# Optimization experiments

Hardware: AMD Instinct MI355X
Metric: run time of the kernel (lower is better)

The kernel has to match this reference:

```python
import jax, jax.numpy as jnp
import numpy as np

N = 50000          # nodes
E = 1_600_000      # edges (avg degree 32)
F = 64             # num_features
IN = 8             # in_channels per band
BANDS = F // IN    # 8 band passes
H = 2              # heads
C = 16             # mid_channels (per-head dim)
HC = H * C         # 32
GIN = HC * BANDS   # 256, GCNConv input dim
OUT = 32           # out_channels
ELU_ALPHA = 0.1


def setup_inputs() -> dict:
    key = jax.random.key(0)
    ks = jax.random.split(key, 12)
    s = 0.05
    inp = {
        "x": jax.random.normal(ks[0], (N, F), jnp.float32),
        "edge_attrs": jax.random.uniform(ks[1], (E, 2), jnp.float32),
        # TransformerConv linear layers (shared across all band passes)
        "Wq": jax.random.normal(ks[2], (IN, HC), jnp.float32) * s,
        "bq": jnp.zeros((HC,), jnp.float32),
        "Wk": jax.random.normal(ks[3], (IN, HC), jnp.float32) * s,
        "bk": jnp.zeros((HC,), jnp.float32),
        "Wv": jax.random.normal(ks[4], (IN, HC), jnp.float32) * s,
        "bv": jnp.zeros((HC,), jnp.float32),
        "We": jax.random.normal(ks[5], (2, HC), jnp.float32) * s,   # lin_edge, no bias
        "Wskip": jax.random.normal(ks[6], (IN, HC), jnp.float32) * s,
        "bskip": jnp.zeros((HC,), jnp.float32),
        # final GCNConv (improved=True)
        "Wg": jax.random.normal(ks[7], (GIN, OUT), jnp.float32) * s,
        "bg": jnp.zeros((OUT,), jnp.float32),
        "edge_index": jax.random.randint(ks[8], (2, E), 0, N, jnp.int32),
    }
    return inp


def reference(x, edge_attrs, Wq, bq, Wk, bk, Wv, bv, We, Wskip, bskip, Wg, bg, edge_index):
    src, dst = edge_index[0], edge_index[1]
    inv_sqrt_c = 1.0 / jnp.sqrt(jnp.float32(C))

    # edge embedding is band-independent; compute once
    e = (edge_attrs @ We).reshape(E, H, C)

    def band_pass(xi):  # xi: [N, IN]
        q = (xi @ Wq + bq).reshape(N, H, C)
        k = (xi @ Wk + bk).reshape(N, H, C)
        v = (xi @ Wv + bv).reshape(N, H, C)
        kj = k[src] + e                                   # [E,H,C]
        logits = jnp.einsum('ehc,ehc->eh', q[dst], kj) * inv_sqrt_c
        # segment softmax over incoming edges of each dst node
        m = jax.ops.segment_max(logits, dst, num_segments=N)
        m = jnp.where(jnp.isfinite(m), m, 0.0)
        p = jnp.exp(logits - m[dst])
        z = jax.ops.segment_sum(p, dst, num_segments=N)
        alpha = p / (z[dst] + 1e-16)                      # [E,H]
        msg = (v[src] + e) * alpha[:, :, None]            # [E,H,C]
        agg = jax.ops.segment_sum(msg, dst, num_segments=N).reshape(N, HC)
        out = agg + xi @ Wskip + bskip                    # root/skip connection
        # GraphMid applies ELU(alpha=0.1) after the conv
        return jnp.where(out > 0, out, ELU_ALPHA * (jnp.exp(out) - 1.0))

    xb = x.reshape(N, BANDS, IN)
    h = jax.vmap(band_pass, in_axes=1, out_axes=1)(xb).reshape(N, GIN)

    # GCNConv(improved=True) with edge_weight = edge_attrs[:, 1]
    w = edge_attrs[:, 1]
    loops = jnp.arange(N, dtype=src.dtype)
    row = jnp.concatenate([src, loops])
    col = jnp.concatenate([dst, loops])
    ww = jnp.concatenate([w, jnp.full((N,), 2.0, jnp.float32)])  # improved: fill=2
    deg = jax.ops.segment_sum(ww, col, num_segments=N)
    dis = jnp.where(deg > 0, jax.lax.rsqrt(deg), 0.0)
    norm = dis[row] * ww * dis[col]                       # [E+N]
    hw = h @ Wg                                           # [N,OUT]
    out = jax.ops.segment_sum(norm[:, None] * hw[row], col, num_segments=N) + bg
    return out
```

## Files before the change

kernel.cpp:

```cpp
#include <hip/hip_runtime.h>
#include <hip/hip_fp16.h>
#include <math.h>

#define NN 50000
#define NE 1600000
#define F 64
#define H 2
#define C 16
#define HC 32
#define GIN 256
#define OUTC 32
#define PAD 88

#define NPART 196
#define CAPP 9216
#define EPB 8192
#define NB1 196
#define QKV_BLOCKS 1563

static const size_t OFF_QH   = 0;
static const size_t OFF_SH   = (size_t)NN * 128;
static const size_t OFF_KV   = 2 * (size_t)NN * 128;
static const size_t OFF_HWH  = OFF_KV + (size_t)NN * 128;
static const size_t OFF_DIS  = OFF_HWH + (size_t)NN * 16;
static const size_t OFF_CUR  = OFF_DIS + NN;
static const size_t OFF_PCUR = OFF_CUR + NN;
static const size_t OFF_PART = OFF_PCUR + 4096;
static const size_t OFF_PAY  = OFF_PART + (size_t)NPART * CAPP * 2;

typedef _Float16 h2 __attribute__((ext_vector_type(2)));
typedef _Float16 h4 __attribute__((ext_vector_type(4)));
typedef _Float16 h8 __attribute__((ext_vector_type(8)));
typedef float f2 __attribute__((ext_vector_type(2)));
union F4H { float4 f; h2 h[4]; };
union H8U { h8 v; h2 h[4]; };
union I2H { int2 i; h2 h[2]; };

__device__ __forceinline__ float fdot2(h2 a, h2 b, float c) {
#if defined(__has_builtin) && __has_builtin(__builtin_amdgcn_fdot2)
    return __builtin_amdgcn_fdot2(a, b, c, false);
#else
    return c + (float)a.x * (float)b.x + (float)a.y * (float)b.y;
#endif
}

__device__ __forceinline__ h2 dec_lo(unsigned d) {
    union { unsigned u; h2 h; } c;
    c.u = __builtin_amdgcn_perm(d, d, 0x010C000CU);
    return c.h;
}
__device__ __forceinline__ h2 dec_hi(unsigned d) {
    union { unsigned u; h2 h; } c;
    c.u = __builtin_amdgcn_perm(d, d, 0x030C020CU);
    return c.h;
}

#if defined(__has_builtin)
#if __has_builtin(__builtin_amdgcn_cvt_pk_f32_bf8)
#define HAVE_CVT_BF8 1
#endif
#endif

__device__ __forceinline__ f2 bf8_lo(int w) {
#ifdef HAVE_CVT_BF8
    return __builtin_amdgcn_cvt_pk_f32_bf8(w, false);
#else
    h2 hh = dec_lo((unsigned)w);
    float2 f = __half22float2(*(const __half2*)&hh);
    f2 r; r.x = f.x; r.y = f.y; return r;
#endif
}
__device__ __forceinline__ f2 bf8_hi(int w) {
#ifdef HAVE_CVT_BF8
    return __builtin_amdgcn_cvt_pk_f32_bf8(w, true);
#else
    h2 hh = dec_hi((unsigned)w);
    float2 f = __half22float2(*(const __half2*)&hh);
    f2 r; r.x = f.x; r.y = f.y; return r;
#endif
}

__global__ __launch_bounds__(256) void k_init(int* __restrict__ pcur) {
    int t = threadIdx.x;
    for (int i = t; i < 4096; i += 256) pcur[i] = 0;
}

__global__ __launch_bounds__(256) void k_p1(
    const float* __restrict__ x,
    const float* __restrict__ Wq, const float* __restrict__ bq,
    const float* __restrict__ Wk, const float* __restrict__ bk,
    const float* __restrict__ Wv, const float* __restrict__ bv,
    const float* __restrict__ Wskip, const float* __restrict__ bskip,
    __half* __restrict__ Qh, unsigned char* __restrict__ KV8,
    __half* __restrict__ Sh,
    const int* __restrict__ ei, const float* __restrict__ ea,
    int* __restrict__ pcur, int2* __restrict__ partA) {
    __shared__ float xs[32 * F];
    __shared__ int hist[256];
    __shared__ int basep[256];
    int t = threadIdx.x;
    if (blockIdx.x < NB1) {
        hist[t] = 0;
        __syncthreads();
        int e0 = blockIdx.x * EPB + t;
        for (int r = 0; r < EPB / 256; r++) {
            int e = e0 + r * 256;
            if (e < NE) atomicAdd(&hist[ei[NE + e] >> 8], 1);
        }
        __syncthreads();
        {
            int c = hist[t];
            basep[t] = (t < NPART && c > 0) ? atomicAdd(pcur + t * 16, c) : 0;
            hist[t] = 0;
        }
        __syncthreads();
        for (int r = 0; r < EPB / 256; r++) {
            int e = e0 + r * 256;
            if (e < NE) {
                int s = ei[e];
                int d = ei[NE + e];
                float2 a = ((const float2*)ea)[e];
                int bin = d >> 8;
                int loff = atomicAdd(&hist[bin], 1);
                int g = basep[bin] + loff;
                if (g < CAPP) {
                    __half2 eh = __floats2half2_rn(a.x, a.y);
                    int2 rec;
                    rec.x = (s & 0xFFFF) | ((d & 255) << 16);
                    rec.y = *(const int*)&eh;
                    partA[(size_t)bin * CAPP + g] = rec;
                }
            }
        }
        return;
    }
    int base = (blockIdx.x - NB1) * 32;
    for (int i = t; i < 32 * F; i += 256) {
        int node = base + (i >> 6);
        xs[i] = (node < NN) ? x[node * F + (i & 63)] : 0.0f;
    }
    __syncthreads();
    int j = t;
    int band = j >> 5;
    int hc = j & 31;
    float wq[8], wk[8], wv[8], ws[8];
#pragma unroll
    for (int i = 0; i < 8; i++) {
        wq[i] = Wq[i * HC + hc];
        wk[i] = Wk[i * HC + hc];
        wv[i] = Wv[i * HC + hc];
        ws[i] = Wskip[i * HC + hc];
    }
    float bq_ = bq[hc], bk_ = bk[hc], bv_ = bv[hc], bs_ = bskip[hc];
    int bh = j >> 4, ch = j & 15;
    int sub = ch >> 2, pos = ch & 3;
    size_t kvoff = (size_t)bh * 32 + (size_t)sub * 8 + pos;
    for (int nn = 0; nn < 32; nn++) {
        int node = base + nn;
        if (node >= NN) break;
        const float* xr = &xs[nn * F + band * 8];
        float q = bq_, k = bk_, v = bv_, s = bs_;
#pragma unroll
        for (int i = 0; i < 8; i++) {
            float xv = xr[i];
            q += xv * wq[i];
            k += xv * wk[i];
            v += xv * wv[i];
            s += xv * ws[i];
        }
        Qh[(size_t)node * 256 + j] = __float2half(q);
        Sh[(size_t)node * 256 + j] = __float2half(s);
        unsigned ku = __half_as_ushort(__float2half(k));
        unsigned vu = __half_as_ushort(__float2half(v));
        KV8[(size_t)node * 512 + kvoff]     = (unsigned char)((ku + 0x80u) >> 8);
        KV8[(size_t)node * 512 + kvoff + 4] = (unsigned char)((vu + 0x80u) >> 8);
    }
}

__global__ __launch_bounds__(256) void k_p2(
    const int* __restrict__ pcur, const int2* __restrict__ partA,
    int2* __restrict__ pay, int* __restrict__ cur) {
    __shared__ int lcnt[256];
    int p = blockIdx.x;
    int t = threadIdx.x;
    lcnt[t] = 0;
    __syncthreads();
    int nrec = pcur[p * 16];
    if (nrec > CAPP) nrec = CAPP;
    const int2* pb = partA + (size_t)p * CAPP;
    for (int i = t; i < nrec; i += 256) {
        int2 rec = pb[i];
        int s = rec.x & 0xFFFF;
        int d8 = (rec.x >> 16) & 255;
        int pos = atomicAdd(&lcnt[d8], 1);
        if (pos < PAD) {
            int2 pl;
            pl.x = s;
            pl.y = rec.y;
            pay[(size_t)((p << 8) + d8) * PAD + pos] = pl;
        }
    }
    __syncthreads();
    int d = (p << 8) + t;
    if (d < NN) cur[d] = lcnt[t];
}

__global__ __launch_bounds__(256) void k_agg(
    const unsigned char* __restrict__ KV8, const __half* __restrict__ Sh,
    const float* __restrict__ We, const float* __restrict__ Wg,
    const int* __restrict__ cnt, const int2* __restrict__ pay,
    const __half* __restrict__ QH,
    __half* __restrict__ HWh, float* __restrict__ dis) {
    __shared__ __attribute__((aligned(16))) _Float16 wgt[32][264];
    __shared__ __attribute__((aligned(16))) _Float16 hls[4][256];
    int t = threadIdx.x;
    for (int idx = t; idx < GIN * OUTC; idx += 256)
        wgt[idx & 31][idx >> 5] = (_Float16)Wg[idx];

    int wv = t >> 6;
    int n = __builtin_amdgcn_readfirstlane(blockIdx.x * 4 + wv);
    int lane = t & 63;
    int bh = lane >> 2;
    int sub = lane & 3;
    int head = bh & 1;
    int coff = bh * 16 + sub * 4;

    I2H q;
    q.i = *(const int2*)(QH + (size_t)n * 256 + coff);
    q.h[0] = q.h[0] * (_Float16)0.25f;
    q.h[1] = q.h[1] * (_Float16)0.25f;
    float qf[4];
    {
        float2 f0 = __half22float2(*(const __half2*)&q.h[0]);
        float2 f1 = __half22float2(*(const __half2*)&q.h[1]);
        qf[0] = f0.x; qf[1] = f0.y; qf[2] = f1.x; qf[3] = f1.y;
    }
    float we0[4], we1[4];
#pragma unroll
    for (int c = 0; c < 4; c++) {
        we0[c] = We[head * 16 + sub * 4 + c];
        we1[c] = We[32 + head * 16 + sub * 4 + c];
    }
    float qw0 = 0.0f, qw1 = 0.0f;
#pragma unroll
    for (int c = 0; c < 4; c++) {
        qw0 += qf[c] * we0[c];
        qw1 += qf[c] * we1[c];
    }
    qw0 += __shfl_xor(qw0, 1); qw0 += __shfl_xor(qw0, 2);
    qw1 += __shfl_xor(qw1, 1); qw1 += __shfl_xor(qw1, 2);

    int cN = cnt[n];
    if (cN > PAD) cN = PAD;
    int last = (cN > 0) ? cN - 1 : 0;
    const int2* prow = pay + (size_t)n * PAD;

    f2 acc0 = {0.0f, 0.0f}, acc1 = {0.0f, 0.0f}, za = {0.0f, 0.0f};
    float zz = 0.0f, degs = 0.0f;

    int2 pls[4];
#pragma unroll
    for (int j = 0; j < 4; j++) {
        int ix = (j <= last) ? j : last;
        pls[j] = prow[ix];
    }
    for (int i = 0; i < cN; i += 4) {
        int nb = cN - i;
        if (nb > 4) nb = 4;
        int2 raw[4];
        float2 ev[4];
#pragma unroll
        for (int j = 0; j < 4; j++) {
            int src = pls[j].x;
            ev[j] = __half22float2(*(const __half2*)&pls[j].y);
            raw[j] = *(const int2*)(KV8 + (size_t)src * 512 + lane * 8);
        }
#pragma unroll
        for (int j = 0; j < 4; j++) {
            int ix = i + 4 + j;
            ix = (ix <= last) ? ix : last;
            pls[j] = prow[ix];
        }
#pragma unroll
        for (int j = 0; j < 4; j++) {
            if (j < nb) {
                h2 k0 = dec_lo((unsigned)raw[j].x);
                h2 k1 = dec_hi((unsigned)raw[j].x);
                float d = fdot2(k1, q.h[1], fdot2(k0, q.h[0], 0.0f));
                d += __shfl_xor(d, 1);
                d += __shfl_xor(d, 2);
                float p = __expf(d + qw0 * ev[j].x + qw1 * ev[j].y);
                f2 v01 = bf8_lo(raw[j].y);
                f2 v23 = bf8_hi(raw[j].y);
                f2 pp = {p, p};
                acc0 = v01 * pp + acc0;
                acc1 = v23 * pp + acc1;
                f2 ee = {ev[j].x, ev[j].y};
                za = ee * pp + za;
                zz += p;
                degs += ev[j].y;
            }
        }
    }
    float dn = rsqrtf(degs + 2.0f);
    if (lane == 0) dis[n] = dn;
    {
        I2H sv;
        sv.i = *(const int2*)(Sh + (size_t)n * 256 + coff);
        float2 s0 = __half22float2(*(const __half2*)&sv.h[0]);
        float2 s1 = __half22float2(*(const __half2*)&sv.h[1]);
        float s[4] = {s0.x, s0.y, s1.x, s1.y};
        float a[4] = {acc0.x, acc0.y, acc1.x, acc1.y};
        float inv = 1.0f / (zz + 1e-16f);
        h4 hv;
#pragma unroll
        for (int c = 0; c < 4; c++) {
            float val = (a[c] + za.x * we0[c] + za.y * we1[c]) * inv + s[c];
            val = (val > 0.0f) ? val : 0.1f * (__expf(val) - 1.0f);
            hv[c] = (_Float16)val;
        }
        *(h4*)(&hls[wv][coff]) = hv;
    }
    __syncthreads();
    {
        int r = t & 63;
        int o = r >> 1;
        int hf = r & 1;
        const _Float16* wrow = &wgt[o][hf * 128];
        const _Float16* hrow = &hls[wv][hf * 128];
        float ga = 0.0f;
#pragma unroll
        for (int jj = 0; jj < 128; jj += 8) {
            H8U w, hh;
            w.v = *(const h8*)(wrow + jj);
            hh.v = *(const h8*)(hrow + jj);
            ga = fdot2(w.h[0], hh.h[0], ga);
            ga = fdot2(w.h[1], hh.h[1], ga);
            ga = fdot2(w.h[2], hh.h[2], ga);
            ga = fdot2(w.h[3], hh.h[3], ga);
        }
        ga += __shfl_xor(ga, 1);
        if (hf == 0) HWh[(size_t)n * OUTC + o] = __float2half(dn * ga);
    }
}

__global__ __launch_bounds__(256) void k_out(
    const int* __restrict__ cnt, const int2* __restrict__ pay,
    const float* __restrict__ dis, const __half* __restrict__ HWh,
    const float* __restrict__ bg, float* __restrict__ out) {
    int t = threadIdx.x;
    int n = blockIdx.x * 4 + (t >> 6);
    int lane = t & 63;
    int o = lane & 31;
    int sl = lane >> 5;
    int cN = cnt[n];
    if (cN > PAD) cN = PAD;
    int s0i = n * PAD;
    int s1 = s0i + cN;
    int last = (cN > 0) ? s1 - 1 : s0i;
    float acc = 0.0f;
    int i = s0i + sl;
    int2 c0 = pay[(i <= last) ? i : s0i];
    int2 c1 = pay[(i + 2 <= last) ? (i + 2) : s0i];
    for (; i + 2 < s1; i += 4) {
        int2 p0 = c0, p1 = c1;
        int ip0 = i + 4, ip1 = i + 6;
        c0 = pay[(ip0 <= last) ? ip0 : s0i];
        c1 = pay[(ip1 <= last) ? ip1 : s0i];
        float h0 = __half2float(HWh[(size_t)p0.x * OUTC + o]);
        float h1 = __half2float(HWh[(size_t)p1.x * OUTC + o]);
        float2 e0 = __half22float2(*(const __half2*)&p0.y);
        float2 e1 = __half22float2(*(const __half2*)&p1.y);
        acc += e0.y * h0 + e1.y * h1;
    }
    if (i < s1) {
        int2 pl = c0;
        float2 ev = __half22float2(*(const __half2*)&pl.y);
        acc += ev.y * __half2float(HWh[(size_t)pl.x * OUTC + o]);
    }
    acc += __shfl_xor(acc, 32);
    if (sl == 0) {
        float dn = dis[n];
        out[n * OUTC + o] = bg[o] + dn * acc +
                            2.0f * dn * __half2float(HWh[(size_t)n * OUTC + o]);
    }
}

extern "C" void kernel_launch(void* const* d_in, const int* in_sizes, int n_in,
                              void* d_out, int out_size, void* d_ws, size_t ws_size,
                              hipStream_t stream) {
    const float* x = (const float*)d_in[0];
    const float* ea = (const float*)d_in[1];
    const float* Wq = (const float*)d_in[2];
    const float* bq = (const float*)d_in[3];
    const float* Wk = (const float*)d_in[4];
    const float* bk = (const float*)d_in[5];
    const float* Wv = (const float*)d_in[6];
    const float* bv = (const float*)d_in[7];
    const float* We = (const float*)d_in[8];
    const float* Wskip = (const float*)d_in[9];
    const float* bskip = (const float*)d_in[10];
    const float* Wg = (const float*)d_in[11];
    const float* bg = (const float*)d_in[12];
    const int* ei = (const int*)d_in[13];
    float* out = (float*)d_out;
    float* ws = (float*)d_ws;

    __half* QH  = (__half*)(ws + OFF_QH);
    __half* SH  = (__half*)(ws + OFF_SH);
    unsigned char* KV8 = (unsigned char*)(ws + OFF_KV);
    __half* HWH = (__half*)(ws + OFF_HWH);
    float* DIS  = ws + OFF_DIS;
    int* CUR    = (int*)(ws + OFF_CUR);
    int* PCUR   = (int*)(ws + OFF_PCUR);
    int2* PARTA = (int2*)(ws + OFF_PART);
    int2* PAY   = (int2*)(ws + OFF_PAY);

    k_init<<<1, 256, 0, stream>>>(PCUR);
    k_p1<<<NB1 + QKV_BLOCKS, 256, 0, stream>>>(
        x, Wq, bq, Wk, bk, Wv, bv, Wskip, bskip, QH, KV8, SH, ei, ea,
        PCUR, PARTA);
    k_p2<<<NPART, 256, 0, stream>>>(PCUR, PARTA, PAY, CUR);
    k_agg<<<NN / 4, 256, 0, stream>>>(KV8, SH, We, Wg, CUR, PAY, QH, HWH, DIS);
    k_out<<<NN / 4, 256, 0, stream>>>(CUR, PAY, DIS, HWH, bg, out);
}
```

Before: 343.5 us.

## Process four edges per lane-quad in aggregation and split K/V byte layout

```diff
diff --git a/kernel.cpp b/kernel.cpp
--- a/kernel.cpp
+++ b/kernel.cpp
@@ -152,9 +152,6 @@
         ws[i] = Wskip[i * HC + hc];
     }
     float bq_ = bq[hc], bk_ = bk[hc], bv_ = bv[hc], bs_ = bskip[hc];
-    int bh = j >> 4, ch = j & 15;
-    int sub = ch >> 2, pos = ch & 3;
-    size_t kvoff = (size_t)bh * 32 + (size_t)sub * 8 + pos;
     for (int nn = 0; nn < 32; nn++) {
         int node = base + nn;
         if (node >= NN) break;
@@ -172,8 +169,8 @@
         Sh[(size_t)node * 256 + j] = __float2half(s);
         unsigned ku = __half_as_ushort(__float2half(k));
         unsigned vu = __half_as_ushort(__float2half(v));
-        KV8[(size_t)node * 512 + kvoff]     = (unsigned char)((ku + 0x80u) >> 8);
-        KV8[(size_t)node * 512 + kvoff + 4] = (unsigned char)((vu + 0x80u) >> 8);
+        KV8[(size_t)node * 512 + j]       = (unsigned char)((ku + 0x80u) >> 8);
+        KV8[(size_t)node * 512 + 256 + j] = (unsigned char)((vu + 0x80u) >> 8);
     }
 }
 
@@ -223,94 +220,104 @@
     int bh = lane >> 2;
     int sub = lane & 3;
     int head = bh & 1;
-    int coff = bh * 16 + sub * 4;
-
-    I2H q;
-    q.i = *(const int2*)(QH + (size_t)n * 256 + coff);
-    q.h[0] = q.h[0] * (_Float16)0.25f;
-    q.h[1] = q.h[1] * (_Float16)0.25f;
-    float qf[4];
-    {
-        float2 f0 = __half22float2(*(const __half2*)&q.h[0]);
-        float2 f1 = __half22float2(*(const __half2*)&q.h[1]);
-        qf[0] = f0.x; qf[1] = f0.y; qf[2] = f1.x; qf[3] = f1.y;
-    }
-    float we0[4], we1[4];
-#pragma unroll
-    for (int c = 0; c < 4; c++) {
-        we0[c] = We[head * 16 + sub * 4 + c];
-        we1[c] = We[32 + head * 16 + sub * 4 + c];
-    }
+
+    H8U q0, q1;
+    q0.v = *(const h8*)(QH + (size_t)n * 256 + bh * 16);
+    q1.v = *(const h8*)(QH + (size_t)n * 256 + bh * 16 + 8);
+    const h2 qs = {(_Float16)0.25f, (_Float16)0.25f};
+#pragma unroll
+    for (int m = 0; m < 4; m++) { q0.h[m] *= qs; q1.h[m] *= qs; }
+
     float qw0 = 0.0f, qw1 = 0.0f;
 #pragma unroll
-    for (int c = 0; c < 4; c++) {
-        qw0 += qf[c] * we0[c];
-        qw1 += qf[c] * we1[c];
-    }
-    qw0 += __shfl_xor(qw0, 1); qw0 += __shfl_xor(qw0, 2);
-    qw1 += __shfl_xor(qw1, 1); qw1 += __shfl_xor(qw1, 2);
+    for (int m = 0; m < 4; m++) {
+        float2 f0 = __half22float2(*(const __half2*)&q0.h[m]);
+        float2 f1 = __half22float2(*(const __half2*)&q1.h[m]);
+        const float* w0 = We + head * 16;
+        const float* w1 = We + 32 + head * 16;
+        qw0 += f0.x * w0[2 * m] + f0.y * w0[2 * m + 1];
+        qw0 += f1.x * w0[8 + 2 * m] + f1.y * w0[8 + 2 * m + 1];
+        qw1 += f0.x * w1[2 * m] + f0.y * w1[2 * m + 1];
+        qw1 += f1.x * w1[8 + 2 * m] + f1.y * w1[8 + 2 * m + 1];
+    }
 
     int cN = cnt[n];
     if (cN > PAD) cN = PAD;
     int last = (cN > 0) ? cN - 1 : 0;
     const int2* prow = pay + (size_t)n * PAD;
 
-    f2 acc0 = {0.0f, 0.0f}, acc1 = {0.0f, 0.0f}, za = {0.0f, 0.0f};
+    f2 acc0 = {0,0}, acc1 = {0,0}, acc2 = {0,0}, acc3 = {0,0};
+    f2 acc4 = {0,0}, acc5 = {0,0}, acc6 = {0,0}, acc7 = {0,0};
+    f2 za = {0.0f, 0.0f};
     float zz = 0.0f, degs = 0.0f;
 
-    int2 pls[4];
-#pragma unroll
-    for (int j = 0; j < 4; j++) {
-        int ix = (j <= last) ? j : last;
-        pls[j] = prow[ix];
-    }
+    int2 pl = prow[(sub <= last) ? sub : last];
     for (int i = 0; i < cN; i += 4) {
-        int nb = cN - i;
-        if (nb > 4) nb = 4;
-        int2 raw[4];
-        float2 ev[4];
-#pragma unroll
-        for (int j = 0; j < 4; j++) {
-            int src = pls[j].x;
-            ev[j] = __half22float2(*(const __half2*)&pls[j].y);
-            raw[j] = *(const int2*)(KV8 + (size_t)src * 512 + lane * 8);
-        }
-#pragma unroll
-        for (int j = 0; j < 4; j++) {
-            int ix = i + 4 + j;
-            ix = (ix <= last) ? ix : last;
-            pls[j] = prow[ix];
-        }
-#pragma unroll
-        for (int j = 0; j < 4; j++) {
-            if (j < nb) {
-                h2 k0 = dec_lo((unsigned)raw[j].x);
-                h2 k1 = dec_hi((unsigned)raw[j].x);
-                float d = fdot2(k1, q.h[1], fdot2(k0, q.h[0], 0.0f));
-                d += __shfl_xor(d, 1);
-                d += __shfl_xor(d, 2);
-                float p = __expf(d + qw0 * ev[j].x + qw1 * ev[j].y);
-                f2 v01 = bf8_lo(raw[j].y);
-                f2 v23 = bf8_hi(raw[j].y);
-                f2 pp = {p, p};
-                acc0 = v01 * pp + acc0;
-                acc1 = v23 * pp + acc1;
-                f2 ee = {ev[j].x, ev[j].y};
-                za = ee * pp + za;
-                zz += p;
-                degs += ev[j].y;
-            }
-        }
-    }
+        bool ok = (i + sub) < cN;
+        int src = pl.x;
+        float2 ev = __half22float2(*(const __half2*)&pl.y);
+        const unsigned char* kvp = KV8 + (size_t)src * 512 + bh * 16;
+        int4 rk = *(const int4*)kvp;
+        int4 rv = *(const int4*)(kvp + 256);
+        int nix = i + 4 + sub;
+        nix = (nix <= last) ? nix : last;
+        pl = prow[nix];
+        float d = 0.0f;
+        d = fdot2(dec_lo((unsigned)rk.x), q0.h[0], d);
+        d = fdot2(dec_hi((unsigned)rk.x), q0.h[1], d);
+        d = fdot2(dec_lo((unsigned)rk.y), q0.h[2], d);
+        d = fdot2(dec_hi((unsigned)rk.y), q0.h[3], d);
+        d = fdot2(dec_lo((unsigned)rk.z), q1.h[0], d);
+        d = fdot2(dec_hi((unsigned)rk.z), q1.h[1], d);
+        d = fdot2(dec_lo((unsigned)rk.w), q1.h[2], d);
+        d = fdot2(dec_hi((unsigned)rk.w), q1.h[3], d);
+        float logit = d + qw0 * ev.x + qw1 * ev.y;
+        logit = ok ? logit : -1e30f;
+        float p = __expf(logit);
+        float a1 = ok ? ev.y : 0.0f;
+        f2 pp = {p, p};
+        acc0 = bf8_lo(rv.x) * pp + acc0;
+        acc1 = bf8_hi(rv.x) * pp + acc1;
+        acc2 = bf8_lo(rv.y) * pp + acc2;
+        acc3 = bf8_hi(rv.y) * pp + acc3;
+        acc4 = bf8_lo(rv.z) * pp + acc4;
+        acc5 = bf8_hi(rv.z) * pp + acc5;
+        acc6 = bf8_lo(rv.w) * pp + acc6;
+        acc7 = bf8_hi(rv.w) * pp + acc7;
+        f2 ee = {ev.x, ev.y};
+        za = ee * pp + za;
+        zz += p;
+        degs += a1;
+    }
+#define QR(v) v += __shfl_xor(v, 1); v += __shfl_xor(v, 2)
+    QR(acc0.x); QR(acc0.y); QR(acc1.x); QR(acc1.y);
+    QR(acc2.x); QR(acc2.y); QR(acc3.x); QR(acc3.y);
+    QR(acc4.x); QR(acc4.y); QR(acc5.x); QR(acc5.y);
+    QR(acc6.x); QR(acc6.y); QR(acc7.x); QR(acc7.y);
+    QR(za.x); QR(za.y); QR(zz); QR(degs);
+#undef QR
     float dn = rsqrtf(degs + 2.0f);
     if (lane == 0) dis[n] = dn;
     {
+        f2 aaL = (sub & 1) ? acc2 : acc0;
+        f2 aaH = (sub & 1) ? acc3 : acc1;
+        f2 abL = (sub & 1) ? acc6 : acc4;
+        f2 abH = (sub & 1) ? acc7 : acc5;
+        f2 a01 = (sub & 2) ? abL : aaL;
+        f2 a23 = (sub & 2) ? abH : aaH;
+        float a[4] = {a01.x, a01.y, a23.x, a23.y};
+        int coff = bh * 16 + sub * 4;
+        float we0[4], we1[4];
+#pragma unroll
+        for (int c = 0; c < 4; c++) {
+            we0[c] = We[head * 16 + sub * 4 + c];
+            we1[c] = We[32 + head * 16 + sub * 4 + c];
+        }
         I2H sv;
         sv.i = *(const int2*)(Sh + (size_t)n * 256 + coff);
         float2 s0 = __half22float2(*(const __half2*)&sv.h[0]);
         float2 s1 = __half22float2(*(const __half2*)&sv.h[1]);
         float s[4] = {s0.x, s0.y, s1.x, s1.y};
-        float a[4] = {acc0.x, acc0.y, acc1.x, acc1.y};
         float inv = 1.0f / (zz + 1e-16f);
         h4 hv;
 #pragma unroll
```

New measurement: 365.6 us. +6.4%, slower.
